# Performance work log

Hardware: AMD Instinct MI355X
Metric: run time of the kernel (lower is better)

Reference implementation:

```python
import jax, jax.numpy as jnp
import numpy as np

EPS = 1e-13

def masked_softmax(vec, mask, axis=-1):
    # Old AllenNLP masked_softmax: softmax(vec * mask), re-mask, renormalize.
    result = jax.nn.softmax(vec * mask, axis=axis)
    result = result * mask
    return result / (result.sum(axis=axis, keepdims=True) + EPS)

def setup_inputs() -> dict:
    key = jax.random.key(0)
    k1, k2, k3, k4 = jax.random.split(key, 4)
    B, N, T, U, H = 8, 20, 300, 64, 512
    doc_encoding = jax.random.normal(k1, (B, N, T, H), dtype=jnp.float32)
    q_encoding = jax.random.normal(k2, (B, U, H), dtype=jnp.float32)
    doc_mask = jax.random.randint(k3, (B, N, T), 0, 2, dtype=jnp.int32)
    q_mask = jax.random.randint(k4, (B, U), 0, 2, dtype=jnp.int32)
    return {"doc_encoding": doc_encoding, "q_encoding": q_encoding,
            "doc_mask": doc_mask, "q_mask": q_mask}

def reference(doc_encoding, q_encoding, doc_mask, q_mask):
    B, N, T, H = doc_encoding.shape
    U = q_encoding.shape[1]
    dtype = doc_encoding.dtype
    dm = doc_mask.astype(dtype)            # B,N,T
    qm = q_mask.astype(dtype)              # B,U
    doc = doc_encoding.reshape(B, N * T, H)  # B,NT,H
    # shared unnormalized co-attention scores: B,NT,U
    scores = jnp.einsum('bkh,buh->bku', doc, q_encoding)
    # doc->question attention (softmax over U, masked by q_mask)
    attn = masked_softmax(scores, qm[:, None, :], axis=-1)  # B,NT,U
    aggq = jnp.einsum('bku,buh->bkh', attn, q_encoding)      # B,NT,H
    # question->doc attention (softmax over T within each doc, masked by doc_mask)
    attn_t = scores.transpose(0, 2, 1).reshape(B, U, N, T)   # B,U,N,T
    attn_t = masked_softmax(attn_t, dm[:, None, :, :], axis=-1)
    attn_t = attn_t.reshape(B, U, N * T)
    aggdoc = jnp.einsum('buk,bkh->buh', attn_t, doc)          # B,U,H
    aggq2 = jnp.einsum('bku,buh->bkh', attn, aggdoc)          # B,NT,H
    out = jnp.concatenate([aggq.reshape(B, N, T, H),
                           aggq2.reshape(B, N, T, H)], axis=-1)  # B,N,T,2H
    return out
```

## Files before the change

kernel.cpp:

```cpp
#include <hip/hip_runtime.h>

#define BB 8
#define NN 20
#define TT 300
#define UU 64
#define HH 512
#define NT 6000


typedef __attribute__((ext_vector_type(4))) float f32x4;
typedef __attribute__((ext_vector_type(8))) short s16x8;

__device__ __forceinline__ float bf2f(unsigned short u) {
  union { unsigned int i; float f; } c; c.i = ((unsigned int)u) << 16; return c.f;
}
__device__ __forceinline__ unsigned short f2bf(float f) {
  union { float f; unsigned int i; } c; c.f = f;
  unsigned int u = c.i;
  unsigned int r = (u + 0x7fffu + ((u >> 16) & 1u)) >> 16;
  return (unsigned short)r;
}
__device__ __forceinline__ void splitbf(float x, unsigned short& hi, unsigned short& lo) {
  hi = f2bf(x);
  lo = f2bf(x - bf2f(hi));
}
__device__ __forceinline__ f32x4 mfma16(s16x8 a, s16x8 b, f32x4 c) {
  return __builtin_amdgcn_mfma_f32_16x16x32_bf16(a, b, c, 0, 0, 0);
}

__global__ __launch_bounds__(256) void kdetect(const unsigned short* __restrict__ d16,
                                               int* __restrict__ flag) {
  __shared__ int cnt[4];
  int t = threadIdx.x;
  unsigned short v = d16[t];
  int e = (v >> 7) & 0xFF;
  int weird = (e > 140 || (e < 110 && (v & 0x7FFFu) != 0)) ? 1 : 0;
  unsigned long long m = __ballot(weird);
  if ((t & 63) == 0) cnt[t >> 6] = __popcll(m);
  __syncthreads();
  if (t == 0) flag[0] = (cnt[0] + cnt[1] + cnt[2] + cnt[3] >= 32) ? 1 : 0;
}

__global__ __launch_bounds__(256) void k0_init(const void* __restrict__ qv,
                                               const int* __restrict__ flag,
                                               float* __restrict__ W,
                                               unsigned short* __restrict__ QsH,
                                               unsigned short* __restrict__ QsL) {
  const int isf32 = *flag;
  int idx = blockIdx.x * 256 + threadIdx.x;
  int h2 = idx & 1023;
  int bu = idx >> 10;
  float v = 0.0f;
  if (h2 < HH) {
    v = isf32 ? ((const float*)qv)[bu * HH + h2]
              : bf2f(((const unsigned short*)qv)[bu * HH + h2]);
    unsigned short hi, lo;
    splitbf(v, hi, lo);
    QsH[bu * HH + h2] = hi;
    QsL[bu * HH + h2] = lo;
  }
  W[idx] = v;
}

__global__ __launch_bounds__(512) void k1_mfma(const void* __restrict__ docv,
                                               const unsigned short* __restrict__ QsH,
                                               const unsigned short* __restrict__ QsL,
                                               const int* __restrict__ flag,
                                               float* __restrict__ scores) {
  __shared__ __align__(16) unsigned short sDh[128 * 64], sDl[128 * 64];
  const int isf32 = *flag;
  const int b = blockIdx.y, kt = blockIdx.x;
  const int tid = threadIdx.x;
  const int lane = tid & 63, w = tid >> 6;
  const int l15 = lane & 15, l4 = lane >> 4;
  const int kmax = NT - kt * 128;
  const size_t dbase = (size_t)(b * NT + kt * 128) * HH;
  const size_t qrow0 = (size_t)b * UU * HH;
  const f32x4 zero = {0.f, 0.f, 0.f, 0.f};
  f32x4 acc[4] = {zero, zero, zero, zero};

  for (int hc = 0; hc < 8; ++hc) {
    if (hc) __syncthreads();
#pragma unroll
    for (int i = 0; i < 2; ++i) {
      int g = tid + 512 * i;
      int row = g >> 3, h8 = (g & 7) * 8;
      int addr = (row * 128 + h8 * 2) ^ ((row & 7) << 4);
      float v[8] = {0.f, 0.f, 0.f, 0.f, 0.f, 0.f, 0.f, 0.f};
      if (row < kmax) {
        size_t off = dbase + (size_t)row * HH + hc * 64 + h8;
        if (isf32) {
          const float* df = (const float*)docv;
          float4 a0 = *(const float4*)(df + off);
          float4 a1 = *(const float4*)(df + off + 4);
          v[0] = a0.x; v[1] = a0.y; v[2] = a0.z; v[3] = a0.w;
          v[4] = a1.x; v[5] = a1.y; v[6] = a1.z; v[7] = a1.w;
        } else {
          const unsigned short* db = (const unsigned short*)docv;
          ushort4 a0 = *(const ushort4*)(db + off);
          ushort4 a1 = *(const ushort4*)(db + off + 4);
          v[0] = bf2f(a0.x); v[1] = bf2f(a0.y); v[2] = bf2f(a0.z); v[3] = bf2f(a0.w);
          v[4] = bf2f(a1.x); v[5] = bf2f(a1.y); v[6] = bf2f(a1.z); v[7] = bf2f(a1.w);
        }
      }
      s16x8 vh, vl;
#pragma unroll
      for (int j = 0; j < 8; ++j) {
        unsigned short hh, ll; splitbf(v[j], hh, ll);
        vh[j] = (short)hh; vl[j] = (short)ll;
      }
      *(s16x8*)((char*)sDh + addr) = vh;
      *(s16x8*)((char*)sDl + addr) = vl;
    }
    __syncthreads();
    s16x8 qh[2][4], ql[2][4];
#pragma unroll
    for (int kb = 0; kb < 2; ++kb)
#pragma unroll
      for (int mt = 0; mt < 4; ++mt) {
        size_t qa = qrow0 + (size_t)(mt * 16 + l15) * HH + hc * 64 + kb * 32 + l4 * 8;
        qh[kb][mt] = *(const s16x8*)&QsH[qa];
        ql[kb][mt] = *(const s16x8*)&QsL[qa];
      }
#pragma unroll
    for (int kb = 0; kb < 2; ++kb) {
      const int off = kb * 64 + l4 * 16;
      const int brow = w * 16 + l15;
      const int ba = (brow * 128 + off) ^ ((brow & 7) << 4);
      s16x8 bh = *(const s16x8*)((const char*)sDh + ba);
      s16x8 bl = *(const s16x8*)((const char*)sDl + ba);
#pragma unroll
      for (int mt = 0; mt < 4; ++mt) {
        acc[mt] = mfma16(qh[kb][mt], bh, acc[mt]);
        acc[mt] = mfma16(qh[kb][mt], bl, acc[mt]);
        acc[mt] = mfma16(ql[kb][mt], bh, acc[mt]);
      }
    }
  }
  const int krow = w * 16 + l15;
  if (krow < kmax) {
    size_t ro = ((size_t)b * NT + kt * 128 + krow) * 64;
#pragma unroll
    for (int mt = 0; mt < 4; ++mt)
      *(f32x4*)&scores[ro + mt * 16 + l4 * 4] = acc[mt];
  }
}

__global__ __launch_bounds__(256) void k2b_tstats(const float* __restrict__ scores,
                                                  const int* __restrict__ dm,
                                                  float* __restrict__ tmax,
                                                  float* __restrict__ tsum) {
  const int b = blockIdx.x / NN;
  const int n = blockIdx.x % NN;
  const int u = threadIdx.x & 63;
  const int tg = threadIdx.x >> 6;
  float m = -__builtin_inff(), s = 0.0f;
  for (int t = tg; t < TT; t += 4) {
    int dmv = dm[(b * NN + n) * TT + t];
    if (dmv) {
      float v = scores[((size_t)(b * NT) + n * TT + t) * 64 + u];
      if (v > m) { s = s * __expf(m - v) + 1.0f; m = v; }
      else s += __expf(v - m);
    }
  }
  __shared__ float sm[4][64], ss[4][64];
  sm[tg][u] = m; ss[tg][u] = s;
  __syncthreads();
  if (threadIdx.x < 64) {
    float M = sm[0][u];
#pragma unroll
    for (int i = 1; i < 4; ++i) M = fmaxf(M, sm[i][u]);
    float S = 0.0f;
#pragma unroll
    for (int i = 0; i < 4; ++i) {
      if (ss[i][u] > 0.0f) S += ss[i][u] * __expf(sm[i][u] - M);
    }
    tmax[(b * 64 + u) * NN + n] = M;
    tsum[(b * 64 + u) * NN + n] = S;
  }
}

__global__ __launch_bounds__(256) void k2c2(const float* __restrict__ scores,
                                            const int* __restrict__ qm,
                                            const int* __restrict__ dm,
                                            const float* __restrict__ tmax,
                                            const float* __restrict__ tsum,
                                            unsigned short* __restrict__ PaH,
                                            unsigned short* __restrict__ PaL,
                                            unsigned short* __restrict__ Pt) {
  const int row = blockIdx.x * 4 + (threadIdx.x >> 6);
  const int u = threadIdx.x & 63;
  const int b = row / NT;
  const int k = row - b * NT;
  const int n = k / TT;
  const float s = scores[(size_t)row * 64 + u];
  const int m = qm[b * 64 + u];
  float v = m ? s : -__builtin_inff();
#pragma unroll
  for (int o = 32; o > 0; o >>= 1) v = fmaxf(v, __shfl_xor(v, o, 64));
  float e = m ? __expf(s - v) : 0.0f;
  float sum = e;
#pragma unroll
  for (int o = 32; o > 0; o >>= 1) sum += __shfl_xor(sum, o, 64);
  float attn = (sum > 0.0f) ? (e / sum) : 0.0f;
  unsigned short hi, lo;
  splitbf(attn, hi, lo);
  PaH[(size_t)row * 64 + u] = hi;
  PaL[(size_t)row * 64 + u] = lo;
  float wgt = 0.0f;
  if (dm[b * NT + k]) {
    float S = tsum[(b * 64 + u) * NN + n];
    if (S > 0.0f) wgt = __expf(s - tmax[(b * 64 + u) * NN + n]) / S;
  }
  Pt[(size_t)row * 64 + u] = f2bf(wgt);
}

__global__ __launch_bounds__(256) void k3_mfma(const unsigned short* __restrict__ Pt,
                                               const void* __restrict__ docv,
                                               const int* __restrict__ flag,
                                               float* __restrict__ W) {
  __shared__ __align__(16) unsigned short sDh[128 * 64], sDl[128 * 64];
  __shared__ __align__(16) unsigned short sP[64 * 64];
  const int isf32 = *flag;
  const int b = blockIdx.z, hc = blockIdx.y, kc = blockIdx.x;
  const int tid = threadIdx.x, lane = tid & 63, w = tid >> 6;
  const int l15 = lane & 15, l4 = lane >> 4;
  const int k0base = kc * 250, kend = k0base + 250;
  const f32x4 zero = {0.f, 0.f, 0.f, 0.f};
  f32x4 acc[4][2];
#pragma unroll
  for (int mt = 0; mt < 4; ++mt) { acc[mt][0] = zero; acc[mt][1] = zero; }

  for (int kb = k0base; kb < kend; kb += 64) {
    const int kn = min(64, kend - kb);
    if (kb != k0base) __syncthreads();
    {
      const int ug = tid & 15, kg = tid >> 4;
      ushort4 r[4];
#pragma unroll
      for (int rr = 0; rr < 4; ++rr) {
        int kk = kg * 4 + rr;
        ushort4 t = make_ushort4(0, 0, 0, 0);
        if (kk < kn) t = *(const ushort4*)&Pt[((size_t)b * NT + kb + kk) * 64 + ug * 4];
        r[rr] = t;
      }
      const unsigned short* rp = (const unsigned short*)r;
#pragma unroll
      for (int uu = 0; uu < 4; ++uu) {
        int u = ug * 4 + uu;
        int addr = (u * 128 + kg * 8) ^ ((u & 7) << 4);
        ushort4 col = make_ushort4(rp[0 * 4 + uu], rp[1 * 4 + uu], rp[2 * 4 + uu], rp[3 * 4 + uu]);
        *(ushort4*)((char*)sP + addr) = col;
      }
    }
#pragma unroll
    for (int i = 0; i < 2; ++i) {
      int s = tid + 256 * i;
      int hg = s & 31, kg = s >> 5;
      float rv[4][4];
#pragma unroll
      for (int rr = 0; rr < 4; ++rr) {
        int kk = kg * 4 + rr;
        float4 v = make_float4(0.f, 0.f, 0.f, 0.f);
        if (kk < kn) {
          size_t off = ((size_t)b * NT + kb + kk) * HH + hc * 128 + hg * 4;
          if (isf32) v = *(const float4*)((const float*)docv + off);
          else {
            ushort4 t = *(const ushort4*)((const unsigned short*)docv + off);
            v = make_float4(bf2f(t.x), bf2f(t.y), bf2f(t.z), bf2f(t.w));
          }
        }
        rv[rr][0] = v.x; rv[rr][1] = v.y; rv[rr][2] = v.z; rv[rr][3] = v.w;
      }
#pragma unroll
      for (int hh = 0; hh < 4; ++hh) {
        int hrow = hg * 4 + hh;
        int addr = (hrow * 128 + kg * 8) ^ ((hrow & 7) << 4);
        unsigned short h0, l0, h1, l1, h2, l2, h3, l3;
        splitbf(rv[0][hh], h0, l0);
        splitbf(rv[1][hh], h1, l1);
        splitbf(rv[2][hh], h2, l2);
        splitbf(rv[3][hh], h3, l3);
        *(ushort4*)((char*)sDh + addr) = make_ushort4(h0, h1, h2, h3);
        *(ushort4*)((char*)sDl + addr) = make_ushort4(l0, l1, l2, l3);
      }
    }
    __syncthreads();
#pragma unroll
    for (int ks = 0; ks < 2; ++ks) {
      const int off = ks * 64 + l4 * 16;
      s16x8 bh[2], bl[2];
#pragma unroll
      for (int nt = 0; nt < 2; ++nt) {
        int r = w * 32 + nt * 16 + l15;
        int a = (r * 128 + off) ^ ((r & 7) << 4);
        bh[nt] = *(const s16x8*)((const char*)sDh + a);
        bl[nt] = *(const s16x8*)((const char*)sDl + a);
      }
#pragma unroll
      for (int mt = 0; mt < 4; ++mt) {
        int r = mt * 16 + l15;
        int a = (r * 128 + off) ^ ((r & 7) << 4);
        s16x8 pa = *(const s16x8*)((const char*)sP + a);
#pragma unroll
        for (int nt = 0; nt < 2; ++nt) {
          acc[mt][nt] = mfma16(pa, bh[nt], acc[mt][nt]);
          acc[mt][nt] = mfma16(pa, bl[nt], acc[mt][nt]);
        }
      }
    }
  }
#pragma unroll
  for (int mt = 0; mt < 4; ++mt)
#pragma unroll
    for (int nt = 0; nt < 2; ++nt)
#pragma unroll
      for (int j = 0; j < 4; ++j) {
        int u = mt * 16 + l4 * 4 + j;
        int h = hc * 128 + w * 32 + nt * 16 + l15;
        atomicAdd(&W[((size_t)b * 64 + u) * 1024 + 512 + h], acc[mt][nt][j]);
      }
}

__global__ __launch_bounds__(256) void k35_wt(const float* __restrict__ W,
                                              unsigned short* __restrict__ WtH,
                                              unsigned short* __restrict__ WtL) {
  __shared__ float sW[64][68];
  const int b = blockIdx.y, hck = blockIdx.x;
  const int tid = threadIdx.x;
#pragma unroll
  for (int i = 0; i < 4; ++i) {
    int g = tid + 256 * i;
    int u = g >> 4, c4 = (g & 15) * 4;
    *(float4*)&sW[u][c4] = *(const float4*)&W[((size_t)b * 64 + u) * 1024 + hck * 64 + c4];
  }
  __syncthreads();
  const int h = tid >> 2, ug = tid & 3;
  s16x8 oh[2], ol[2];
#pragma unroll
  for (int p = 0; p < 2; ++p)
#pragma unroll
    for (int j = 0; j < 8; ++j) {
      unsigned short hh, ll;
      splitbf(sW[ug * 16 + p * 8 + j][h], hh, ll);
      oh[p][j] = (short)hh; ol[p][j] = (short)ll;
    }
  size_t ob = ((size_t)b * 1024 + hck * 64 + h) * 64 + ug * 16;
  *(s16x8*)&WtH[ob] = oh[0];
  *(s16x8*)&WtH[ob + 8] = oh[1];
  *(s16x8*)&WtL[ob] = ol[0];
  *(s16x8*)&WtL[ob + 8] = ol[1];
}

__global__ __launch_bounds__(256) void k4_mfma(const unsigned short* __restrict__ PaH,
                                               const unsigned short* __restrict__ PaL,
                                               const unsigned short* __restrict__ WtH,
                                               const unsigned short* __restrict__ WtL,
                                               const int* __restrict__ flag,
                                               void* __restrict__ outv) {
  const int isf32 = *flag;
  const int b = blockIdx.z, ht = blockIdx.y, kt = blockIdx.x;
  const int tid = threadIdx.x, lane = tid & 63, w = tid >> 6;
  const int l15 = lane & 15, l4 = lane >> 4;
  const int h0 = ht * 64;
  const int kr0 = kt * 256 + w * 64;
  const f32x4 zero = {0.f, 0.f, 0.f, 0.f};
  f32x4 acc[4][4];
#pragma unroll
  for (int mt = 0; mt < 4; ++mt)
#pragma unroll
    for (int nt = 0; nt < 4; ++nt) acc[mt][nt] = zero;
#pragma unroll
  for (int kb = 0; kb < 2; ++kb) {
    s16x8 ah[4], al[4];
#pragma unroll
    for (int mt = 0; mt < 4; ++mt) {
      size_t a = ((size_t)b * 1024 + h0 + mt * 16 + l15) * 64 + kb * 32 + l4 * 8;
      ah[mt] = *(const s16x8*)&WtH[a];
      al[mt] = *(const s16x8*)&WtL[a];
    }
#pragma unroll
    for (int nt = 0; nt < 4; ++nt) {
      int krow = kr0 + nt * 16 + l15;
      int krc = krow < NT ? krow : NT - 1;
      size_t pb = ((size_t)b * NT + krc) * 64 + kb * 32 + l4 * 8;
      s16x8 bh = *(const s16x8*)&PaH[pb];
      s16x8 bl = *(const s16x8*)&PaL[pb];
#pragma unroll
      for (int mt = 0; mt < 4; ++mt) {
        acc[mt][nt] = mfma16(ah[mt], bh, acc[mt][nt]);
        acc[mt][nt] = mfma16(ah[mt], bl, acc[mt][nt]);
        acc[mt][nt] = mfma16(al[mt], bh, acc[mt][nt]);
      }
    }
  }
#pragma unroll
  for (int nt = 0; nt < 4; ++nt) {
    int krow = kr0 + nt * 16 + l15;
    if (krow < NT) {
      size_t ob = ((size_t)b * NT + krow) * 1024 + h0;
#pragma unroll
      for (int mt = 0; mt < 4; ++mt) {
        int h2 = mt * 16 + l4 * 4;
        if (isf32) {
          *(f32x4*)((float*)outv + ob + h2) = acc[mt][nt];
        } else {
          ushort4 o;
          o.x = f2bf(acc[mt][nt][0]); o.y = f2bf(acc[mt][nt][1]);
          o.z = f2bf(acc[mt][nt][2]); o.w = f2bf(acc[mt][nt][3]);
          *(ushort4*)((unsigned short*)outv + ob + h2) = o;
        }
      }
    }
  }
}

__global__ __launch_bounds__(256) void k2_softmax_u(float* __restrict__ scores,
                                                    const int* __restrict__ qm) {
  const int row = blockIdx.x * 4 + (threadIdx.x >> 6);
  const int u = threadIdx.x & 63;
  const int b = row / NT;
  const float s = scores[(size_t)row * 64 + u];
  const int m = qm[b * 64 + u];
  float v = m ? s : -__builtin_inff();
#pragma unroll
  for (int o = 32; o > 0; o >>= 1) v = fmaxf(v, __shfl_xor(v, o, 64));
  float e = m ? __expf(s - v) : 0.0f;
  float sum = e;
#pragma unroll
  for (int o = 32; o > 0; o >>= 1) sum += __shfl_xor(sum, o, 64);
  scores[(size_t)row * 64 + u] = (sum > 0.0f) ? (e / sum) : 0.0f;
}

__global__ __launch_bounds__(256) void k3_aggdoc(const float* __restrict__ scores,
                                                 const void* __restrict__ docv,
                                                 const int* __restrict__ dm,
                                                 const float* __restrict__ tmax,
                                                 const float* __restrict__ tsum,
                                                 const int* __restrict__ flag,
                                                 float* __restrict__ W) {
  __shared__ float wL[32][68];
  __shared__ float dL[32][68];
  const int isf32 = *flag;
  const int b = blockIdx.z, hc = blockIdx.y, kc = blockIdx.x;
  const int tid = threadIdx.x;
  const int th = tid & 15, tuq = tid >> 4;
  float acc[4][4] = {};
  const int k0base = kc * 375, kend = k0base + 375;
  for (int k0 = k0base; k0 < kend; k0 += 32) {
    const int kn = min(32, kend - k0);
#pragma unroll
    for (int i = 0; i < 8; ++i) {
      int idx = tid + 256 * i;
      int kk = idx >> 6, uu = idx & 63;
      float wv = 0.0f;
      if (kk < kn) {
        int k = k0 + kk;
        int n = k / TT;
        if (dm[b * NT + k]) {
          float S = tsum[(b * 64 + uu) * NN + n];
          if (S > 0.0f) {
            float M = tmax[(b * 64 + uu) * NN + n];
            wv = __expf(scores[((size_t)(b * NT) + k) * 64 + uu] - M) / S;
          }
        }
      }
      wL[kk][uu] = wv;
    }
#pragma unroll
    for (int i = 0; i < 2; ++i) {
      int g = tid + 256 * i;
      int kk = g >> 4, c4 = (g & 15) * 4;
      float4 v = make_float4(0.f, 0.f, 0.f, 0.f);
      if (kk < kn) {
        size_t off = ((size_t)(b * NT) + k0 + kk) * HH + hc * 64 + c4;
        if (isf32) v = *(const float4*)((const float*)docv + off);
        else {
          ushort4 t4 = *(const ushort4*)((const unsigned short*)docv + off);
          v = make_float4(bf2f(t4.x), bf2f(t4.y), bf2f(t4.z), bf2f(t4.w));
        }
      }
      *(float4*)&dL[kk][c4] = v;
    }
    __syncthreads();
    for (int kk = 0; kk < kn; ++kk) {
      float4 w4 = *(const float4*)&wL[kk][tuq * 4];
      float4 d4 = *(const float4*)&dL[kk][th * 4];
      acc[0][0] += w4.x * d4.x; acc[0][1] += w4.x * d4.y; acc[0][2] += w4.x * d4.z; acc[0][3] += w4.x * d4.w;
      acc[1][0] += w4.y * d4.x; acc[1][1] += w4.y * d4.y; acc[1][2] += w4.y * d4.z; acc[1][3] += w4.y * d4.w;
      acc[2][0] += w4.z * d4.x; acc[2][1] += w4.z * d4.y; acc[2][2] += w4.z * d4.z; acc[2][3] += w4.z * d4.w;
      acc[3][0] += w4.w * d4.x; acc[3][1] += w4.w * d4.y; acc[3][2] += w4.w * d4.z; acc[3][3] += w4.w * d4.w;
    }
    __syncthreads();
  }
#pragma unroll
  for (int i = 0; i < 4; ++i) {
#pragma unroll
    for (int j = 0; j < 4; ++j) {
      size_t addr = ((size_t)(b * 64) + tuq * 4 + i) * 1024 + 512 + hc * 64 + th * 4 + j;
      atomicAdd(&W[addr], acc[i][j]);
    }
  }
}

__global__ __launch_bounds__(256) void k4_out(const float* __restrict__ attn,
                                              const float* __restrict__ W,
                                              const int* __restrict__ flag,
                                              void* __restrict__ outv) {
  __shared__ float sAt[64][68];
  __shared__ float sWt[64][132];
  const int isf32 = *flag;
  const int b = blockIdx.z;
  const int kt = blockIdx.x;
  const int ht = blockIdx.y;
  const int tid = threadIdx.x;
  const int th2 = tid & 15, tkq = tid >> 4;
#pragma unroll
  for (int i = 0; i < 4; ++i) {
    int g = tid + 256 * i;
    int row = g >> 4, c4 = (g & 15) * 4;
    int k = kt * 64 + row;
    float4 v = make_float4(0.f, 0.f, 0.f, 0.f);
    if (k < NT) v = *(const float4*)&attn[((size_t)(b * NT) + k) * 64 + c4];
    *(float4*)&sAt[row][c4] = v;
  }
#pragma unroll
  for (int i = 0; i < 8; ++i) {
    int g = tid + 256 * i;
    int row = g >> 5, c4 = (g & 31) * 4;
    float4 wv = *(const float4*)&W[((size_t)(b * 64) + row) * 1024 + ht * 128 + c4];
    *(float4*)&sWt[row][c4] = wv;
  }
  __syncthreads();
  float acc[4][8] = {};
#pragma unroll 4
  for (int u = 0; u < 64; u += 4) {
    float a[4][4];
#pragma unroll
    for (int i = 0; i < 4; ++i)
      *(float4*)a[i] = *(const float4*)&sAt[tkq * 4 + i][u];
#pragma unroll
    for (int r = 0; r < 4; ++r) {
      float4 w0 = *(const float4*)&sWt[u + r][th2 * 4];
      float4 w1 = *(const float4*)&sWt[u + r][64 + th2 * 4];
#pragma unroll
      for (int i = 0; i < 4; ++i) {
        acc[i][0] += a[i][r] * w0.x; acc[i][1] += a[i][r] * w0.y;
        acc[i][2] += a[i][r] * w0.z; acc[i][3] += a[i][r] * w0.w;
        acc[i][4] += a[i][r] * w1.x; acc[i][5] += a[i][r] * w1.y;
        acc[i][6] += a[i][r] * w1.z; acc[i][7] += a[i][r] * w1.w;
      }
    }
  }
#pragma unroll
  for (int i = 0; i < 4; ++i) {
    int k = kt * 64 + tkq * 4 + i;
    if (k < NT) {
      size_t off = ((size_t)(b * NT) + k) * 1024 + ht * 128 + th2 * 4;
      if (isf32) {
        *(float4*)((float*)outv + off) = make_float4(acc[i][0], acc[i][1], acc[i][2], acc[i][3]);
        *(float4*)((float*)outv + off + 64) = make_float4(acc[i][4], acc[i][5], acc[i][6], acc[i][7]);
      } else {
        ushort4 o0, o1;
        o0.x = f2bf(acc[i][0]); o0.y = f2bf(acc[i][1]); o0.z = f2bf(acc[i][2]); o0.w = f2bf(acc[i][3]);
        o1.x = f2bf(acc[i][4]); o1.y = f2bf(acc[i][5]); o1.z = f2bf(acc[i][6]); o1.w = f2bf(acc[i][7]);
        *(ushort4*)((unsigned short*)outv + off) = o0;
        *(ushort4*)((unsigned short*)outv + off + 64) = o1;
      }
    }
  }
}

extern "C" void kernel_launch(void* const* d_in, const int* in_sizes, int n_in,
                              void* d_out, int out_size, void* d_ws, size_t ws_size,
                              hipStream_t stream) {
  const void* doc = d_in[0];
  const void* q   = d_in[1];
  const int* dmask = (const int*)d_in[2];
  const int* qmask = (const int*)d_in[3];

  float* ws = (float*)d_ws;
  float* scores = ws;
  float* tmax   = ws + 3072000;
  float* tsum   = ws + 3082240;
  float* W      = ws + 3092480;
  int*   flag   = (int*)(ws + 3616768);
  unsigned short* QsH = (unsigned short*)(ws + 3616772);
  unsigned short* QsL = (unsigned short*)(ws + 3747844);
  unsigned short* Pt  = (unsigned short*)(ws + 3878916);
  unsigned short* PaH = (unsigned short*)(ws + 5414916);
  unsigned short* PaL = (unsigned short*)(ws + 6950916);
  unsigned short* WtH = (unsigned short*)(ws + 8486916);
  unsigned short* WtL = (unsigned short*)(ws + 8749060);
  const size_t need_new = (size_t)9011204 * 4;

  kdetect<<<1, 256, 0, stream>>>((const unsigned short*)doc, flag);
  k0_init<<<2048, 256, 0, stream>>>(q, flag, W, QsH, QsL);
  k1_mfma<<<dim3(47, 8), 512, 0, stream>>>(doc, QsH, QsL, flag, scores);
  k2b_tstats<<<160, 256, 0, stream>>>(scores, dmask, tmax, tsum);
  if (ws_size >= need_new) {
    k2c2<<<12000, 256, 0, stream>>>(scores, qmask, dmask, tmax, tsum, PaH, PaL, Pt);
    k3_mfma<<<dim3(24, 4, 8), 256, 0, stream>>>(Pt, doc, flag, W);
    k35_wt<<<dim3(16, 8), 256, 0, stream>>>(W, WtH, WtL);
    k4_mfma<<<dim3(24, 16, 8), 256, 0, stream>>>(PaH, PaL, WtH, WtL, flag, d_out);
  } else {
    k3_aggdoc<<<dim3(16, 8, 8), 256, 0, stream>>>(scores, doc, dmask, tmax, tsum, flag, W);
    k2_softmax_u<<<12000, 256, 0, stream>>>(scores, qmask);
    k4_out<<<dim3(94, 8, 8), 256, 0, stream>>>(scores, W, flag, d_out);
  }
}
```

Before: 444.8 us.

## Inline dtype detection per kernel, stage Q in LDS for scores GEMM, widen tstats

Removes the separate single-block detect kernel. Each kernel now recomputes the fp32/bf16 flag with a wave-level shuffle reduction over the first 256 halfwords of doc, which saves one launch and a dependent global load. The scores GEMM kernel moves from 128-row tiles with 512 threads to 64-row tiles with 256 threads, and stages the Q hi/lo tiles in LDS instead of having every wave load them from global into registers. The T-statistics kernel uses 512 threads to split the T loop eight ways. The costs are redundant detection work in every block and a smaller doc reuse tile per block in the scores GEMM.

```diff
diff --git a/kernel.cpp b/kernel.cpp
--- a/kernel.cpp
+++ b/kernel.cpp
@@ -28,25 +28,27 @@
   return __builtin_amdgcn_mfma_f32_16x16x32_bf16(a, b, c, 0, 0, 0);
 }
 
-__global__ __launch_bounds__(256) void kdetect(const unsigned short* __restrict__ d16,
-                                               int* __restrict__ flag) {
-  __shared__ int cnt[4];
-  int t = threadIdx.x;
-  unsigned short v = d16[t];
-  int e = (v >> 7) & 0xFF;
-  int weird = (e > 140 || (e < 110 && (v & 0x7FFFu) != 0)) ? 1 : 0;
-  unsigned long long m = __ballot(weird);
-  if ((t & 63) == 0) cnt[t >> 6] = __popcll(m);
-  __syncthreads();
-  if (t == 0) flag[0] = (cnt[0] + cnt[1] + cnt[2] + cnt[3] >= 32) ? 1 : 0;
+__device__ __forceinline__ int detect_isf32(const void* docv) {
+  const unsigned short* d16 = (const unsigned short*)docv;
+  int l = threadIdx.x & 63;
+  int cnt = 0;
+#pragma unroll
+  for (int j = 0; j < 4; ++j) {
+    unsigned short v = d16[l * 4 + j];
+    int e = (v >> 7) & 0xFF;
+    cnt += (e > 140 || (e < 110 && (v & 0x7FFFu) != 0)) ? 1 : 0;
+  }
+#pragma unroll
+  for (int o = 32; o > 0; o >>= 1) cnt += __shfl_xor(cnt, o, 64);
+  return cnt >= 32;
 }
 
 __global__ __launch_bounds__(256) void k0_init(const void* __restrict__ qv,
-                                               const int* __restrict__ flag,
+                                               const void* __restrict__ docv,
                                                float* __restrict__ W,
                                                unsigned short* __restrict__ QsH,
                                                unsigned short* __restrict__ QsL) {
-  const int isf32 = *flag;
+  const int isf32 = detect_isf32(docv);
   int idx = blockIdx.x * 256 + threadIdx.x;
   int h2 = idx & 1023;
   int bu = idx >> 10;
@@ -62,20 +64,20 @@
   W[idx] = v;
 }
 
-__global__ __launch_bounds__(512) void k1_mfma(const void* __restrict__ docv,
+__global__ __launch_bounds__(256) void k1_mfma(const void* __restrict__ docv,
                                                const unsigned short* __restrict__ QsH,
                                                const unsigned short* __restrict__ QsL,
-                                               const int* __restrict__ flag,
                                                float* __restrict__ scores) {
-  __shared__ __align__(16) unsigned short sDh[128 * 64], sDl[128 * 64];
-  const int isf32 = *flag;
+  __shared__ __align__(16) unsigned short sDh[64 * 64], sDl[64 * 64];
+  __shared__ __align__(16) unsigned short sQh[64 * 64], sQl[64 * 64];
+  const int isf32 = detect_isf32(docv);
   const int b = blockIdx.y, kt = blockIdx.x;
   const int tid = threadIdx.x;
   const int lane = tid & 63, w = tid >> 6;
   const int l15 = lane & 15, l4 = lane >> 4;
-  const int kmax = NT - kt * 128;
-  const size_t dbase = (size_t)(b * NT + kt * 128) * HH;
-  const size_t qrow0 = (size_t)b * UU * HH;
+  const int kmax = NT - kt * 64;
+  const size_t dbase = (size_t)(b * NT + kt * 64) * HH;
+  const size_t qbase = (size_t)b * UU * HH;
   const f32x4 zero = {0.f, 0.f, 0.f, 0.f};
   f32x4 acc[4] = {zero, zero, zero, zero};
 
@@ -83,7 +85,7 @@
     if (hc) __syncthreads();
 #pragma unroll
     for (int i = 0; i < 2; ++i) {
-      int g = tid + 512 * i;
+      int g = tid + 256 * i;
       int row = g >> 3, h8 = (g & 7) * 8;
       int addr = (row * 128 + h8 * 2) ^ ((row & 7) << 4);
       float v[8] = {0.f, 0.f, 0.f, 0.f, 0.f, 0.f, 0.f, 0.f};
@@ -112,16 +114,16 @@
       *(s16x8*)((char*)sDh + addr) = vh;
       *(s16x8*)((char*)sDl + addr) = vl;
     }
+#pragma unroll
+    for (int i = 0; i < 2; ++i) {
+      int g = tid + 256 * i;
+      int row = g >> 3, h8 = (g & 7) * 8;
+      int addr = (row * 128 + h8 * 2) ^ ((row & 7) << 4);
+      size_t off = qbase + (size_t)row * HH + hc * 64 + h8;
+      *(s16x8*)((char*)sQh + addr) = *(const s16x8*)&QsH[off];
+      *(s16x8*)((char*)sQl + addr) = *(const s16x8*)&QsL[off];
+    }
     __syncthreads();
-    s16x8 qh[2][4], ql[2][4];
-#pragma unroll
-    for (int kb = 0; kb < 2; ++kb)
-#pragma unroll
-      for (int mt = 0; mt < 4; ++mt) {
-        size_t qa = qrow0 + (size_t)(mt * 16 + l15) * HH + hc * 64 + kb * 32 + l4 * 8;
-        qh[kb][mt] = *(const s16x8*)&QsH[qa];
-        ql[kb][mt] = *(const s16x8*)&QsL[qa];
-      }
 #pragma unroll
     for (int kb = 0; kb < 2; ++kb) {
       const int off = kb * 64 + l4 * 16;
@@ -131,22 +133,26 @@
       s16x8 bl = *(const s16x8*)((const char*)sDl + ba);
 #pragma unroll
       for (int mt = 0; mt < 4; ++mt) {
-        acc[mt] = mfma16(qh[kb][mt], bh, acc[mt]);
-        acc[mt] = mfma16(qh[kb][mt], bl, acc[mt]);
-        acc[mt] = mfma16(ql[kb][mt], bh, acc[mt]);
+        const int arow = mt * 16 + l15;
+        const int aa = (arow * 128 + off) ^ ((arow & 7) << 4);
+        s16x8 ah = *(const s16x8*)((const char*)sQh + aa);
+        s16x8 al = *(const s16x8*)((const char*)sQl + aa);
+        acc[mt] = mfma16(ah, bh, acc[mt]);
+        acc[mt] = mfma16(ah, bl, acc[mt]);
+        acc[mt] = mfma16(al, bh, acc[mt]);
       }
     }
   }
   const int krow = w * 16 + l15;
   if (krow < kmax) {
-    size_t ro = ((size_t)b * NT + kt * 128 + krow) * 64;
+    size_t ro = ((size_t)b * NT + kt * 64 + krow) * 64;
 #pragma unroll
     for (int mt = 0; mt < 4; ++mt)
       *(f32x4*)&scores[ro + mt * 16 + l4 * 4] = acc[mt];
   }
 }
 
-__global__ __launch_bounds__(256) void k2b_tstats(const float* __restrict__ scores,
+__global__ __launch_bounds__(512) void k2b_tstats(const float* __restrict__ scores,
                                                   const int* __restrict__ dm,
                                                   float* __restrict__ tmax,
                                                   float* __restrict__ tsum) {
@@ -155,7 +161,7 @@
   const int u = threadIdx.x & 63;
   const int tg = threadIdx.x >> 6;
   float m = -__builtin_inff(), s = 0.0f;
-  for (int t = tg; t < TT; t += 4) {
+  for (int t = tg; t < TT; t += 8) {
     int dmv = dm[(b * NN + n) * TT + t];
     if (dmv) {
       float v = scores[((size_t)(b * NT) + n * TT + t) * 64 + u];
@@ -163,16 +169,16 @@
       else s += __expf(v - m);
     }
   }
-  __shared__ float sm[4][64], ss[4][64];
+  __shared__ float sm[8][64], ss[8][64];
   sm[tg][u] = m; ss[tg][u] = s;
   __syncthreads();
   if (threadIdx.x < 64) {
     float M = sm[0][u];
 #pragma unroll
-    for (int i = 1; i < 4; ++i) M = fmaxf(M, sm[i][u]);
+    for (int i = 1; i < 8; ++i) M = fmaxf(M, sm[i][u]);
     float S = 0.0f;
 #pragma unroll
-    for (int i = 0; i < 4; ++i) {
+    for (int i = 0; i < 8; ++i) {
       if (ss[i][u] > 0.0f) S += ss[i][u] * __expf(sm[i][u] - M);
     }
     tmax[(b * 64 + u) * NN + n] = M;
@@ -217,11 +223,10 @@
 
 __global__ __launch_bounds__(256) void k3_mfma(const unsigned short* __restrict__ Pt,
                                                const void* __restrict__ docv,
-                                               const int* __restrict__ flag,
                                                float* __restrict__ W) {
   __shared__ __align__(16) unsigned short sDh[128 * 64], sDl[128 * 64];
   __shared__ __align__(16) unsigned short sP[64 * 64];
-  const int isf32 = *flag;
+  const int isf32 = detect_isf32(docv);
   const int b = blockIdx.z, hc = blockIdx.y, kc = blockIdx.x;
   const int tid = threadIdx.x, lane = tid & 63, w = tid >> 6;
   const int l15 = lane & 15, l4 = lane >> 4;
@@ -356,9 +361,9 @@
                                                const unsigned short* __restrict__ PaL,
                                                const unsigned short* __restrict__ WtH,
                                                const unsigned short* __restrict__ WtL,
-                                               const int* __restrict__ flag,
+                                               const void* __restrict__ docv,
                                                void* __restrict__ outv) {
-  const int isf32 = *flag;
+  const int isf32 = detect_isf32(docv);
   const int b = blockIdx.z, ht = blockIdx.y, kt = blockIdx.x;
   const int tid = threadIdx.x, lane = tid & 63, w = tid >> 6;
   const int l15 = lane & 15, l4 = lane >> 4;
@@ -437,11 +442,10 @@
                                                  const int* __restrict__ dm,
                                                  const float* __restrict__ tmax,
                                                  const float* __restrict__ tsum,
-                                                 const int* __restrict__ flag,
                                                  float* __restrict__ W) {
   __shared__ float wL[32][68];
   __shared__ float dL[32][68];
-  const int isf32 = *flag;
+  const int isf32 = detect_isf32(docv);
   const int b = blockIdx.z, hc = blockIdx.y, kc = blockIdx.x;
   const int tid = threadIdx.x;
   const int th = tid & 15, tuq = tid >> 4;
@@ -505,11 +509,11 @@
 
 __global__ __launch_bounds__(256) void k4_out(const float* __restrict__ attn,
                                               const float* __restrict__ W,
-                                              const int* __restrict__ flag,
+                                              const void* __restrict__ docv,
                                               void* __restrict__ outv) {
   __shared__ float sAt[64][68];
   __shared__ float sWt[64][132];
-  const int isf32 = *flag;
+  const int isf32 = detect_isf32(docv);
   const int b = blockIdx.z;
   const int kt = blockIdx.x;
   const int ht = blockIdx.y;
@@ -584,7 +588,6 @@
   float* tmax   = ws + 3072000;
   float* tsum   = ws + 3082240;
   float* W      = ws + 3092480;
-  int*   flag   = (int*)(ws + 3616768);
   unsigned short* QsH = (unsigned short*)(ws + 3616772);
   unsigned short* QsL = (unsigned short*)(ws + 3747844);
   unsigned short* Pt  = (unsigned short*)(ws + 3878916);
@@ -594,18 +597,17 @@
   unsigned short* WtL = (unsigned short*)(ws + 8749060);
   const size_t need_new = (size_t)9011204 * 4;
 
-  kdetect<<<1, 256, 0, stream>>>((const unsigned short*)doc, flag);
-  k0_init<<<2048, 256, 0, stream>>>(q, flag, W, QsH, QsL);
-  k1_mfma<<<dim3(47, 8), 512, 0, stream>>>(doc, QsH, QsL, flag, scores);
-  k2b_tstats<<<160, 256, 0, stream>>>(scores, dmask, tmax, tsum);
+  k0_init<<<2048, 256, 0, stream>>>(q, doc, W, QsH, QsL);
+  k1_mfma<<<dim3(94, 8), 256, 0, stream>>>(doc, QsH, QsL, scores);
+  k2b_tstats<<<160, 512, 0, stream>>>(scores, dmask, tmax, tsum);
   if (ws_size >= need_new) {
     k2c2<<<12000, 256, 0, stream>>>(scores, qmask, dmask, tmax, tsum, PaH, PaL, Pt);
-    k3_mfma<<<dim3(24, 4, 8), 256, 0, stream>>>(Pt, doc, flag, W);
+    k3_mfma<<<dim3(24, 4, 8), 256, 0, stream>>>(Pt, doc, W);
     k35_wt<<<dim3(16, 8), 256, 0, stream>>>(W, WtH, WtL);
-    k4_mfma<<<dim3(24, 16, 8), 256, 0, stream>>>(PaH, PaL, WtH, WtL, flag, d_out);
+    k4_mfma<<<dim3(24, 16, 8), 256, 0, stream>>>(PaH, PaL, WtH, WtL, doc, d_out);
   } else {
-    k3_aggdoc<<<dim3(16, 8, 8), 256, 0, stream>>>(scores, doc, dmask, tmax, tsum, flag, W);
+    k3_aggdoc<<<dim3(16, 8, 8), 256, 0, stream>>>(scores, doc, dmask, tmax, tsum, W);
     k2_softmax_u<<<12000, 256, 0, stream>>>(scores, qmask);
-    k4_out<<<dim3(94, 8, 8), 256, 0, stream>>>(scores, W, flag, d_out);
-  }
-}
+    k4_out<<<dim3(94, 8, 8), 256, 0, stream>>>(scores, W, doc, d_out);
+  }
+}
```

New measurement: 398.5 us. -10.4%, faster.
